# Kernel optimization log

Measured on AMD Instinct MI355X. Metric: run time of the kernel, lower is better.

The kernel has to match this reference:

```python
import jax, jax.numpy as jnp
import numpy as np

MASK_VALUE = -1e30


def setup_inputs() -> dict:
    key = jax.random.key(0)
    ks = jax.random.split(key, 8)
    B, N, M, D = 64, 1024, 128, 256
    c = jax.random.normal(ks[0], (B, N, D), dtype=jnp.float32)
    q = jax.random.normal(ks[1], (B, M, D), dtype=jnp.float32)
    c_mask = jax.random.randint(ks[2], (B, N), 0, 2, dtype=jnp.int32)
    q_mask = jax.random.randint(ks[3], (B, M), 0, 2, dtype=jnp.int32)
    w0 = jax.random.normal(ks[4], (D, 1), dtype=jnp.float32) * 0.06  # glorot-ish scale
    w1 = jax.random.normal(ks[5], (D, 1), dtype=jnp.float32) * 0.06
    wm = jax.random.normal(ks[6], (D,), dtype=jnp.float32) * 0.06
    bias = jnp.zeros((M,), dtype=jnp.float32)
    return {"c": c, "q": q, "c_mask": c_mask, "q_mask": q_mask,
            "w0": w0, "w1": w1, "wm": wm, "bias": bias}


def reference(c, q, c_mask, q_mask, w0, w1, wm, bias):
    # Trilinear similarity S[b,i,j] = c.w0 + q.w1 + sum_d c*wm*q + bias[j]
    sub0 = jnp.einsum('bnd,do->bno', c, w0)              # (B,N,1)
    sub1 = jnp.einsum('bmd,do->bom', q, w1)              # (B,1,M)
    sub2 = jnp.einsum('bnd,d,bmd->bnm', c, wm, q)        # (B,N,M)
    S = sub0 + sub1 + sub2 + bias                        # bias broadcast over last axis
    qm = q_mask.astype(jnp.float32)[:, None, :]          # (B,1,M)
    cm = c_mask.astype(jnp.float32)[:, :, None]          # (B,N,1)
    S_ = jax.nn.softmax(S + MASK_VALUE * (1.0 - qm), axis=-1)   # row softmax over query
    S_T = jnp.swapaxes(jax.nn.softmax(S + MASK_VALUE * (1.0 - cm), axis=1), 1, 2)  # (B,M,N)
    c2q = jnp.matmul(S_, q)                              # (B,N,D)
    q2c = jnp.matmul(jnp.matmul(S_, S_T), c)             # (B,N,D)
    return jnp.concatenate([c, c2q, c * c2q, c * q2c], axis=-1)  # (B,N,4D)
```

## Files before the change

kernel.cpp:

```cpp
#include <hip/hip_runtime.h>
#include <cfloat>

#define BB 64
#define NN 1024
#define MM 128
#define DD 256
#define MASKV (-1e30f)

typedef __attribute__((ext_vector_type(8))) short bf16x8;
typedef __attribute__((ext_vector_type(16))) float f32x16;

__device__ __forceinline__ unsigned short f2bf(float x) {
  union { float f; unsigned int u; } v; v.f = x;
  unsigned int r = v.u + 0x7fffu + ((v.u >> 16) & 1u);
  return (unsigned short)(r >> 16);
}
__device__ __forceinline__ float bf2f(unsigned short h) {
  union { float f; unsigned int u; } v; v.u = ((unsigned int)h) << 16;
  return v.f;
}
__device__ __forceinline__ void split8(const float* xs, uint4* hv, uint4* lv) {
  unsigned hp[4], lp[4];
  #pragma unroll
  for (int p = 0; p < 4; p++) {
    unsigned short h0 = f2bf(xs[2 * p]), h1 = f2bf(xs[2 * p + 1]);
    unsigned short g0 = f2bf(xs[2 * p] - bf2f(h0));
    unsigned short g1 = f2bf(xs[2 * p + 1] - bf2f(h1));
    hp[p] = (unsigned)h0 | ((unsigned)h1 << 16);
    lp[p] = (unsigned)g0 | ((unsigned)g1 << 16);
  }
  *hv = make_uint4(hp[0], hp[1], hp[2], hp[3]);
  *lv = make_uint4(lp[0], lp[1], lp[2], lp[3]);
}

__global__ __launch_bounds__(256) void k_dots(
    const float* __restrict__ c, const float* __restrict__ q,
    const int* __restrict__ qmask,
    const float* __restrict__ w0, const float* __restrict__ w1,
    const float* __restrict__ bias,
    float* __restrict__ sub0, float* __restrict__ qtermM) {
  int wave = (blockIdx.x * blockDim.x + threadIdx.x) >> 6;
  int lane = threadIdx.x & 63;
  const int total = BB * NN + BB * MM;
  if (wave >= total) return;
  const float* row;
  const float* w;
  if (wave < BB * NN) { row = c + (size_t)wave * DD; w = w0; }
  else                { row = q + (size_t)(wave - BB * NN) * DD; w = w1; }
  float4 v  = *(const float4*)(row + lane * 4);
  float4 wv = *(const float4*)(w   + lane * 4);
  float s = v.x * wv.x + v.y * wv.y + v.z * wv.z + v.w * wv.w;
  #pragma unroll
  for (int off = 32; off > 0; off >>= 1) s += __shfl_xor(s, off, 64);
  if (lane == 0) {
    if (wave < BB * NN) {
      sub0[wave] = s;
    } else {
      int r = wave - BB * NN;
      int m = r & (MM - 1);
      qtermM[r] = s + bias[m] + (qmask[r] ? 0.0f : MASKV);
    }
  }
}

__global__ __launch_bounds__(256) void k_zero(float* __restrict__ p) {
  p[blockIdx.x * 256 + threadIdx.x] = 0.0f;
}

__global__ __launch_bounds__(256) void k_score(
    const float* __restrict__ c, const float* __restrict__ q,
    const int* __restrict__ cmask, const float* __restrict__ wm,
    const float* __restrict__ sub0, const float* __restrict__ qtermM,
    float* __restrict__ S_, float* __restrict__ E,
    float* __restrict__ colsum) {
  __shared__ unsigned short cwh[128 * 64];
  __shared__ unsigned short cwl[128 * 64];
  __shared__ unsigned short qhi[128 * 64];
  __shared__ unsigned short qlo[128 * 64];
  const int b = blockIdx.y;
  const int n0 = blockIdx.x * 128;
  const int t = threadIdx.x;
  const int w = t >> 6;
  const int l = t & 63;
  const int l31 = l & 31;
  const int lh = l >> 5;

  f32x16 acc[4];
  #pragma unroll
  for (int mb = 0; mb < 4; mb++)
    #pragma unroll
    for (int i = 0; i < 16; i++) acc[mb][i] = 0.0f;

  for (int k0 = 0; k0 < DD; k0 += 64) {
    __syncthreads();
    #pragma unroll
    for (int g = 0; g < 4; g++) {
      int lin = t + g * 256;
      int row = lin >> 3;
      int kg  = (lin & 7) * 8;
      unsigned boff = (unsigned)(row * 128 + ((kg * 2) ^ ((row & 7) << 4)));
      float4 w0v = *(const float4*)(wm + k0 + kg);
      float4 w1v = *(const float4*)(wm + k0 + kg + 4);
      const float* cp = c + (size_t)(b * NN + n0 + row) * DD + k0 + kg;
      float4 a0 = *(const float4*)cp;
      float4 a1 = *(const float4*)(cp + 4);
      float xs[8] = {a0.x * w0v.x, a0.y * w0v.y, a0.z * w0v.z, a0.w * w0v.w,
                     a1.x * w1v.x, a1.y * w1v.y, a1.z * w1v.z, a1.w * w1v.w};
      uint4 hv, lv;
      split8(xs, &hv, &lv);
      *(uint4*)((char*)cwh + boff) = hv;
      *(uint4*)((char*)cwl + boff) = lv;
      const float* qp = q + (size_t)(b * MM + row) * DD + k0 + kg;
      float4 b0 = *(const float4*)qp;
      float4 b1 = *(const float4*)(qp + 4);
      float ys[8] = {b0.x, b0.y, b0.z, b0.w, b1.x, b1.y, b1.z, b1.w};
      split8(ys, &hv, &lv);
      *(uint4*)((char*)qhi + boff) = hv;
      *(uint4*)((char*)qlo + boff) = lv;
    }
    __syncthreads();
    #pragma unroll
    for (int ks = 0; ks < 64; ks += 16) {
      int ak = ks + lh * 8;
      unsigned arow = (unsigned)(w * 32 + l31);
      unsigned aoff = arow * 128 + (((unsigned)(ak * 2)) ^ ((arow & 7) << 4));
      bf16x8 ah = *(const bf16x8*)((const char*)cwh + aoff);
      bf16x8 al = *(const bf16x8*)((const char*)cwl + aoff);
      #pragma unroll
      for (int mb = 0; mb < 4; mb++) {
        unsigned brow = (unsigned)(mb * 32 + l31);
        unsigned boff2 = brow * 128 + (((unsigned)(ak * 2)) ^ ((brow & 7) << 4));
        bf16x8 bh = *(const bf16x8*)((const char*)qhi + boff2);
        bf16x8 bl = *(const bf16x8*)((const char*)qlo + boff2);
        acc[mb] = __builtin_amdgcn_mfma_f32_32x32x16_bf16(ah, bh, acc[mb], 0, 0, 0);
        acc[mb] = __builtin_amdgcn_mfma_f32_32x32x16_bf16(ah, bl, acc[mb], 0, 0, 0);
        acc[mb] = __builtin_amdgcn_mfma_f32_32x32x16_bf16(al, bh, acc[mb], 0, 0, 0);
      }
    }
  }

  float qt[4];
  #pragma unroll
  for (int mb = 0; mb < 4; mb++) qt[mb] = qtermM[b * MM + mb * 32 + l31];

  float ps[4] = {0.f, 0.f, 0.f, 0.f};
  #pragma unroll
  for (int r = 0; r < 16; r++) {
    int row = (r & 3) + 8 * (r >> 2) + 4 * lh;
    int gn = n0 + w * 32 + row;
    float s0m = sub0[b * NN + gn] + (cmask[b * NN + gn] ? 0.0f : MASKV);
    float x[4];
    float vmax = -FLT_MAX;
    #pragma unroll
    for (int mb = 0; mb < 4; mb++) { x[mb] = acc[mb][r] + qt[mb]; vmax = fmaxf(vmax, x[mb]); }
    #pragma unroll
    for (int off = 16; off > 0; off >>= 1) vmax = fmaxf(vmax, __shfl_xor(vmax, off, 64));
    float e[4];
    float vsum = 0.0f;
    #pragma unroll
    for (int mb = 0; mb < 4; mb++) { e[mb] = __expf(x[mb] - vmax); vsum += e[mb]; }
    #pragma unroll
    for (int off = 16; off > 0; off >>= 1) vsum += __shfl_xor(vsum, off, 64);
    float inv = 1.0f / vsum;
    size_t base = (size_t)(b * NN + gn) * MM + l31;
    #pragma unroll
    for (int mb = 0; mb < 4; mb++) {
      S_[base + mb * 32] = e[mb] * inv;
      float Ev = __expf(acc[mb][r] + s0m);
      E[base + mb * 32] = Ev;
      ps[mb] += Ev;
    }
  }
  #pragma unroll
  for (int mb = 0; mb < 4; mb++) {
    ps[mb] += __shfl_xor(ps[mb], 32, 64);
    if (lh == 0) atomicAdd(&colsum[b * MM + mb * 32 + l31], ps[mb]);
  }
}

__global__ __launch_bounds__(256) void k_colA(
    const float* __restrict__ E, const float* __restrict__ c,
    const float* __restrict__ colsum, float* __restrict__ A) {
  __shared__ float se[32 * 64];
  __shared__ float sc[32 * 64];
  const int b = blockIdx.z;
  const int m0 = blockIdx.x * 64;
  const int d0 = blockIdx.y * 64;
  const int t = threadIdx.x;
  const int tx = t & 15;
  const int ty = t >> 4;
  const int lr = t >> 4;
  const int lc = (t & 15) * 4;

  const float* Eb = E + (size_t)b * NN * MM + m0 + lc;
  const float* cb = c + (size_t)b * NN * DD + d0 + lc;

  float4 ev0 = *(const float4*)(Eb + (size_t)lr * MM);
  float4 ev1 = *(const float4*)(Eb + (size_t)(16 + lr) * MM);
  float4 cv0 = *(const float4*)(cb + (size_t)lr * DD);
  float4 cv1 = *(const float4*)(cb + (size_t)(16 + lr) * DD);

  float acc[4][4];
  #pragma unroll
  for (int mi = 0; mi < 4; mi++)
    #pragma unroll
    for (int di = 0; di < 4; di++) acc[mi][di] = 0.0f;

  for (int n0 = 0; n0 < NN; n0 += 32) {
    *(float4*)(&se[lr * 64 + lc])        = ev0;
    *(float4*)(&se[(16 + lr) * 64 + lc]) = ev1;
    *(float4*)(&sc[lr * 64 + lc])        = cv0;
    *(float4*)(&sc[(16 + lr) * 64 + lc]) = cv1;
    __syncthreads();
    if (n0 + 32 < NN) {
      int nn = n0 + 32;
      ev0 = *(const float4*)(Eb + (size_t)(nn + lr) * MM);
      ev1 = *(const float4*)(Eb + (size_t)(nn + 16 + lr) * MM);
      cv0 = *(const float4*)(cb + (size_t)(nn + lr) * DD);
      cv1 = *(const float4*)(cb + (size_t)(nn + 16 + lr) * DD);
    }
    #pragma unroll
    for (int kk = 0; kk < 32; kk++) {
      float4 e4 = *(const float4*)(&se[kk * 64 + ty * 4]);
      float4 c4 = *(const float4*)(&sc[kk * 64 + tx * 4]);
      float em[4] = {e4.x, e4.y, e4.z, e4.w};
      float cd[4] = {c4.x, c4.y, c4.z, c4.w};
      #pragma unroll
      for (int mi = 0; mi < 4; mi++)
        #pragma unroll
        for (int di = 0; di < 4; di++) acc[mi][di] += em[mi] * cd[di];
    }
    __syncthreads();
  }

  #pragma unroll
  for (int mi = 0; mi < 4; mi++) {
    int m = m0 + ty * 4 + mi;
    float inv = 1.0f / colsum[b * MM + m];
    float4 o = make_float4(acc[mi][0] * inv, acc[mi][1] * inv,
                           acc[mi][2] * inv, acc[mi][3] * inv);
    *(float4*)(A + (size_t)(b * MM + m) * DD + d0 + tx * 4) = o;
  }
}

__global__ __launch_bounds__(256) void k_out(
    const float* __restrict__ c, const float* __restrict__ q,
    const float* __restrict__ S_, const float* __restrict__ A,
    float* __restrict__ out) {
  __shared__ float s[32 * 128];
  const int b = blockIdx.y;
  const int n0 = blockIdx.x * 32;
  const int t = threadIdx.x;
  const int dx = t & 63, ry = t >> 6;

  size_t sbase = (size_t)(b * NN + n0) * MM;
  #pragma unroll
  for (int it = 0; it < 16; it++) {
    int idx = t + it * 256;
    s[idx] = S_[sbase + idx];
  }
  __syncthreads();

  float c2q[8][4], q2c[8][4];
  #pragma unroll
  for (int i = 0; i < 8; i++)
    #pragma unroll
    for (int k = 0; k < 4; k++) { c2q[i][k] = 0.f; q2c[i][k] = 0.f; }

  for (int m = 0; m < MM; m++) {
    float4 qv = *(const float4*)(q + (size_t)(b * MM + m) * DD + dx * 4);
    float4 av = *(const float4*)(A + (size_t)(b * MM + m) * DD + dx * 4);
    #pragma unroll
    for (int i = 0; i < 8; i++) {
      float sv = s[(ry * 8 + i) * 128 + m];
      c2q[i][0] += sv * qv.x; c2q[i][1] += sv * qv.y;
      c2q[i][2] += sv * qv.z; c2q[i][3] += sv * qv.w;
      q2c[i][0] += sv * av.x; q2c[i][1] += sv * av.y;
      q2c[i][2] += sv * av.z; q2c[i][3] += sv * av.w;
    }
  }

  #pragma unroll
  for (int i = 0; i < 8; i++) {
    int gn = n0 + ry * 8 + i;
    float4 cv = *(const float4*)(c + (size_t)(b * NN + gn) * DD + dx * 4);
    size_t ob = (size_t)(b * NN + gn) * (4 * DD) + dx * 4;
    float4 o1 = make_float4(c2q[i][0], c2q[i][1], c2q[i][2], c2q[i][3]);
    float4 o2 = make_float4(cv.x * o1.x, cv.y * o1.y, cv.z * o1.z, cv.w * o1.w);
    float4 o3 = make_float4(cv.x * q2c[i][0], cv.y * q2c[i][1],
                            cv.z * q2c[i][2], cv.w * q2c[i][3]);
    *(float4*)(out + ob)            = cv;
    *(float4*)(out + ob + DD)       = o1;
    *(float4*)(out + ob + 2 * DD)   = o2;
    *(float4*)(out + ob + 3 * DD)   = o3;
  }
}

extern "C" void kernel_launch(void* const* d_in, const int* in_sizes, int n_in,
                              void* d_out, int out_size, void* d_ws, size_t ws_size,
                              hipStream_t stream) {
  const float* c     = (const float*)d_in[0];
  const float* q     = (const float*)d_in[1];
  const int*   cmask = (const int*)d_in[2];
  const int*   qmask = (const int*)d_in[3];
  const float* w0    = (const float*)d_in[4];
  const float* w1    = (const float*)d_in[5];
  const float* wm    = (const float*)d_in[6];
  const float* bias  = (const float*)d_in[7];
  float* out = (float*)d_out;
  float* ws  = (float*)d_ws;

  float* S_     = ws;
  float* E      = ws + 8388608;
  float* A      = ws + 16777216;
  float* sub0   = ws + 18874368;
  float* qtermM = ws + 18939904;
  float* colsum = ws + 18948096;

  k_dots<<<18432, 256, 0, stream>>>(c, q, qmask, w0, w1, bias, sub0, qtermM);
  k_zero<<<32, 256, 0, stream>>>(colsum);
  k_score<<<dim3(8, BB), 256, 0, stream>>>(c, q, cmask, wm, sub0, qtermM, S_, E, colsum);
  k_colA<<<dim3(2, 4, BB), 256, 0, stream>>>(E, c, colsum, A);
  k_out<<<dim3(32, BB), 256, 0, stream>>>(c, q, S_, A, out);
}
```

Baseline: 528.2 us.

## Rewrite k_out to use bf16x3 split MFMA for c2q and q2c products

Replaces the scalar FMA outer-product loop in k_out with 32x32x16 bf16 MFMA instructions, splitting each fp32 operand into high and low bf16 parts and issuing three MFMAs to approximate fp32 accuracy. Blocks grow to 512 threads and 64 rows. One group of four waves computes c2q from q and the other computes q2c from A, with operands loaded directly from global memory without shared-memory staging. This aims to cut the ALU-bound matmul cost, but the output stores become scalar and strided, and the B operand loads are strided across DD, which may hurt memory efficiency.

```diff
diff --git a/kernel.cpp b/kernel.cpp
--- a/kernel.cpp
+++ b/kernel.cpp
@@ -31,6 +31,9 @@
   }
   *hv = make_uint4(hp[0], hp[1], hp[2], hp[3]);
   *lv = make_uint4(lp[0], lp[1], lp[2], lp[3]);
+}
+__device__ __forceinline__ bf16x8 u2b(uint4 u) {
+  union { uint4 a; bf16x8 b; } x; x.a = u; return x.b;
 }
 
 __global__ __launch_bounds__(256) void k_dots(
@@ -243,56 +246,73 @@
   }
 }
 
-__global__ __launch_bounds__(256) void k_out(
+__global__ __launch_bounds__(512) void k_out(
     const float* __restrict__ c, const float* __restrict__ q,
     const float* __restrict__ S_, const float* __restrict__ A,
     float* __restrict__ out) {
-  __shared__ float s[32 * 128];
   const int b = blockIdx.y;
-  const int n0 = blockIdx.x * 32;
+  const int n0 = blockIdx.x * 64;
   const int t = threadIdx.x;
-  const int dx = t & 63, ry = t >> 6;
-
-  size_t sbase = (size_t)(b * NN + n0) * MM;
-  #pragma unroll
-  for (int it = 0; it < 16; it++) {
-    int idx = t + it * 256;
-    s[idx] = S_[sbase + idx];
-  }
-  __syncthreads();
-
-  float c2q[8][4], q2c[8][4];
-  #pragma unroll
-  for (int i = 0; i < 8; i++)
-    #pragma unroll
-    for (int k = 0; k < 4; k++) { c2q[i][k] = 0.f; q2c[i][k] = 0.f; }
-
-  for (int m = 0; m < MM; m++) {
-    float4 qv = *(const float4*)(q + (size_t)(b * MM + m) * DD + dx * 4);
-    float4 av = *(const float4*)(A + (size_t)(b * MM + m) * DD + dx * 4);
-    #pragma unroll
-    for (int i = 0; i < 8; i++) {
-      float sv = s[(ry * 8 + i) * 128 + m];
-      c2q[i][0] += sv * qv.x; c2q[i][1] += sv * qv.y;
-      c2q[i][2] += sv * qv.z; c2q[i][3] += sv * qv.w;
-      q2c[i][0] += sv * av.x; q2c[i][1] += sv * av.y;
-      q2c[i][2] += sv * av.z; q2c[i][3] += sv * av.w;
-    }
-  }
-
-  #pragma unroll
-  for (int i = 0; i < 8; i++) {
-    int gn = n0 + ry * 8 + i;
-    float4 cv = *(const float4*)(c + (size_t)(b * NN + gn) * DD + dx * 4);
-    size_t ob = (size_t)(b * NN + gn) * (4 * DD) + dx * 4;
-    float4 o1 = make_float4(c2q[i][0], c2q[i][1], c2q[i][2], c2q[i][3]);
-    float4 o2 = make_float4(cv.x * o1.x, cv.y * o1.y, cv.z * o1.z, cv.w * o1.w);
-    float4 o3 = make_float4(cv.x * q2c[i][0], cv.y * q2c[i][1],
-                            cv.z * q2c[i][2], cv.w * q2c[i][3]);
-    *(float4*)(out + ob)            = cv;
-    *(float4*)(out + ob + DD)       = o1;
-    *(float4*)(out + ob + 2 * DD)   = o2;
-    *(float4*)(out + ob + 3 * DD)   = o3;
+  const int w = t >> 6;
+  const int l = t & 63;
+  const int l31 = l & 31;
+  const int lh = l >> 5;
+  const int grp = w >> 2;
+  const int wi = w & 3;
+  const int nf = wi & 1;
+  const int fd0 = (wi >> 1) * 4;
+
+  const float* Bsrc = grp ? A : q;
+
+  f32x16 acc[4];
+  #pragma unroll
+  for (int df = 0; df < 4; df++)
+    #pragma unroll
+    for (int i = 0; i < 16; i++) acc[df][i] = 0.0f;
+
+  const float* srow = S_ + (size_t)(b * NN + n0 + nf * 32 + l31) * MM + lh * 8;
+  const float* bbase = Bsrc + (size_t)(b * MM + lh * 8) * DD + l31;
+
+  #pragma unroll 2
+  for (int ks = 0; ks < 8; ks++) {
+    float4 s0 = *(const float4*)(srow + ks * 16);
+    float4 s1 = *(const float4*)(srow + ks * 16 + 4);
+    float xs[8] = {s0.x, s0.y, s0.z, s0.w, s1.x, s1.y, s1.z, s1.w};
+    uint4 hv, lv;
+    split8(xs, &hv, &lv);
+    bf16x8 ah = u2b(hv), al = u2b(lv);
+    #pragma unroll
+    for (int df = 0; df < 4; df++) {
+      const float* bp = bbase + (size_t)(ks * 16) * DD + (fd0 + df) * 32;
+      float ys[8];
+      #pragma unroll
+      for (int j = 0; j < 8; j++) ys[j] = bp[j * DD];
+      split8(ys, &hv, &lv);
+      bf16x8 bh = u2b(hv), bl = u2b(lv);
+      acc[df] = __builtin_amdgcn_mfma_f32_32x32x16_bf16(ah, bh, acc[df], 0, 0, 0);
+      acc[df] = __builtin_amdgcn_mfma_f32_32x32x16_bf16(ah, bl, acc[df], 0, 0, 0);
+      acc[df] = __builtin_amdgcn_mfma_f32_32x32x16_bf16(al, bh, acc[df], 0, 0, 0);
+    }
+  }
+
+  #pragma unroll
+  for (int df = 0; df < 4; df++) {
+    int d = (fd0 + df) * 32 + l31;
+    #pragma unroll
+    for (int r = 0; r < 16; r++) {
+      int row = (r & 3) + 8 * (r >> 2) + 4 * lh;
+      int gn = n0 + nf * 32 + row;
+      float v = acc[df][r];
+      float cv = c[(size_t)(b * NN + gn) * DD + d];
+      size_t ob = (size_t)(b * NN + gn) * (4 * DD) + d;
+      if (grp == 0) {
+        out[ob]            = cv;
+        out[ob + DD]       = v;
+        out[ob + 2 * DD]   = cv * v;
+      } else {
+        out[ob + 3 * DD]   = cv * v;
+      }
+    }
   }
 }
 
@@ -321,5 +341,5 @@
   k_zero<<<32, 256, 0, stream>>>(colsum);
   k_score<<<dim3(8, BB), 256, 0, stream>>>(c, q, cmask, wm, sub0, qtermM, S_, E, colsum);
   k_colA<<<dim3(2, 4, BB), 256, 0, stream>>>(E, c, colsum, A);
-  k_out<<<dim3(32, BB), 256, 0, stream>>>(c, q, S_, A, out);
-}
+  k_out<<<dim3(16, BB), 512, 0, stream>>>(c, q, S_, A, out);
+}
```

Measured after the change: 509.1 us. 1.04x faster.
